# Performance work log

Hardware: AMD Instinct MI355X
Metric: run time of the kernel (lower is better)

The kernel has to match this reference:

```python
import jax, jax.numpy as jnp
import numpy as np

D_MODEL, D_FF, H, DK, DV = 1024, 4096, 16, 64, 64
B, S = 16, 512
EPS = 1e-6

def layer_norm(x, g, b):
    mu = jnp.mean(x, axis=-1, keepdims=True)
    var = jnp.var(x, axis=-1, keepdims=True)
    return (x - mu) / jnp.sqrt(var + EPS) * g + b

def setup_inputs() -> dict:
    key = jax.random.key(0)
    ks = jax.random.split(key, 16)
    def lin(k, fan_in, fan_out):
        lim = 1.0 / np.sqrt(fan_in)
        kw, kb = jax.random.split(k)
        W = jax.random.uniform(kw, (fan_in, fan_out), jnp.float32, -lim, lim)
        b = jax.random.uniform(kb, (fan_out,), jnp.float32, -lim, lim)
        return W, b
    Wq, bq = lin(ks[0], D_MODEL, DK * H)
    Wk, bk = lin(ks[1], D_MODEL, DK * H)
    Wv, bv = lin(ks[2], D_MODEL, DV * H)
    Wo, bo = lin(ks[3], DV * H, D_MODEL)
    w1, b1 = lin(ks[4], D_MODEL, D_FF)   # conv1d k=1 == pointwise linear
    w2, b2 = lin(ks[5], D_FF, D_MODEL)
    return {
        "enc_inputs": jax.random.normal(ks[6], (B, S, D_MODEL), jnp.float32),
        "Wq": Wq, "bq": bq, "Wk": Wk, "bk": bk, "Wv": Wv, "bv": bv,
        "Wo": Wo, "bo": bo,
        "ln1_g": jnp.ones((D_MODEL,), jnp.float32), "ln1_b": jnp.zeros((D_MODEL,), jnp.float32),
        "w1": w1, "b1": b1, "w2": w2, "b2": b2,
        "ln2_g": jnp.ones((D_MODEL,), jnp.float32), "ln2_b": jnp.zeros((D_MODEL,), jnp.float32),
        "mask": jax.random.randint(ks[7], (B, S), 0, 2, jnp.int32),
        "max_neighbors": S,
    }

def reference(enc_inputs, Wq, bq, Wk, bk, Wv, bv, Wo, bo, ln1_g, ln1_b,
              w1, b1, w2, b2, ln2_g, ln2_b, mask, max_neighbors):
    x = enc_inputs  # [B, S, D]
    residual = x
    # projections -> [B, H, S, d]
    q = (x @ Wq + bq).reshape(B, S, H, DK).transpose(0, 2, 1, 3)
    k = (x @ Wk + bk).reshape(B, S, H, DK).transpose(0, 2, 1, 3)
    v = (x @ Wv + bv).reshape(B, S, H, DV).transpose(0, 2, 1, 3)
    scores = jnp.einsum('bhqd,bhkd->bhqk', q, k) / np.sqrt(DK)
    pad = (mask == 0)[:, None, None, :]  # [B,1,1,S] broadcasts over heads & query
    scores = jnp.where(pad, jnp.float32(-1e9), scores)
    attn = jax.nn.softmax(scores, axis=-1)
    ctx = jnp.einsum('bhqk,bhkd->bhqd', attn, v)
    ctx = ctx.transpose(0, 2, 1, 3).reshape(B, S, H * DV)
    ctx = ctx @ Wo + bo
    ctx = layer_norm(ctx + residual, ln1_g, ln1_b)
    # position-wise FFN (conv1d kernel=1 == linear)
    ff = jax.nn.relu(ctx @ w1 + b1) @ w2 + b2
    out = layer_norm(ff + ctx, ln2_g, ln2_b)
    return out, attn
```

## Files before the change

kernel.cpp:

```cpp
#include <hip/hip_runtime.h>
#include <hip/hip_bf16.h>

typedef unsigned short u16;
typedef __bf16 bf16x8 __attribute__((ext_vector_type(8)));
typedef float f32x4 __attribute__((ext_vector_type(4)));

static __device__ __forceinline__ float b2f(u16 x) {
    unsigned int u = ((unsigned int)x) << 16;
    float f; __builtin_memcpy(&f, &u, 4); return f;
}
static __device__ __forceinline__ float b2f_u32(unsigned int u) {
    float f; __builtin_memcpy(&f, &u, 4); return f;
}
static __device__ __forceinline__ u16 f2b(float f) {
    unsigned int u; __builtin_memcpy(&u, &f, 4);
    unsigned int lsb = (u >> 16) & 1u;
    u += 0x7fffu + lsb;
    return (u16)(u >> 16);
}

static __device__ __forceinline__ void gload16(const u16* g, u16* l) {
    __builtin_amdgcn_global_load_lds(
        (const __attribute__((address_space(1))) unsigned int*)g,
        (__attribute__((address_space(3))) unsigned int*)l, 16, 0, 0);
}

__global__ __launch_bounds__(256) void transpose_f2b(const float* __restrict__ src,
                                                     u16* __restrict__ dst,
                                                     int R, int C) {
    __shared__ u16 tile[32][33];
    int c0 = blockIdx.x * 32, r0 = blockIdx.y * 32;
    int tx = threadIdx.x & 31, ty = threadIdx.x >> 5;
    for (int i = ty; i < 32; i += 8) {
        int r = r0 + i, c = c0 + tx;
        tile[i][tx] = (r < R && c < C) ? f2b(src[(long)r * C + c]) : (u16)0;
    }
    __syncthreads();
    for (int i = ty; i < 32; i += 8) {
        int c = c0 + i, r = r0 + tx;
        if (c < C && r < R) dst[(long)c * R + r] = tile[tx][i];
    }
}

__global__ __launch_bounds__(256) void concat3(const float* a, const float* b, const float* c,
                                               float* out) {
    int i = blockIdx.x * 256 + threadIdx.x;
    if (i < 1024) out[i] = a[i];
    else if (i < 2048) out[i] = b[i - 1024];
    else if (i < 3072) out[i] = c[i - 2048];
}

__global__ __launch_bounds__(256) void conv_f2b(const float* __restrict__ src,
                                                u16* __restrict__ dst, long n) {
    long i = ((long)blockIdx.x * 256 + threadIdx.x) * 4;
    if (i >= n) return;
    float4 f = *(const float4*)(src + i);
    ushort4 o;
    o.x = f2b(f.x); o.y = f2b(f.y); o.z = f2b(f.z); o.w = f2b(f.w);
    *(ushort4*)(dst + i) = o;
}

#define BM 128
#define BN 128
#define BK 32
__global__ __launch_bounds__(256) void gemm_bt(
    const u16* __restrict__ A, const u16* __restrict__ B,
    const float* __restrict__ bias, u16* __restrict__ C,
    int M, int N, int K, int lda, int ldb, int ldc, int relu) {
    __shared__ __align__(16) u16 As[BM][BK];
    __shared__ __align__(16) u16 Bs[BN][BK];

    int m0 = blockIdx.y * BM;
    int n0 = blockIdx.x * BN;
    int tid = threadIdx.x;
    int lane = tid & 63;
    int wave = tid >> 6;
    int wm = (wave >> 1) * 64;
    int wn = (wave & 1) * 64;
    int lrow = lane & 15;
    int quad = lane >> 4;

    f32x4 acc[4][4];
#pragma unroll
    for (int i = 0; i < 4; i++)
#pragma unroll
        for (int j = 0; j < 4; j++) acc[i][j] = (f32x4){0.f, 0.f, 0.f, 0.f};

    const u16* Arow = A + (long)m0 * lda;
    const u16* Brow = B + (long)n0 * ldb;

    for (int k0 = 0; k0 < K; k0 += BK) {
#pragma unroll
        for (int i = 0; i < 2; i++) {
            int idx = (i * 4 + wave) * 64 + lane;
            int row = idx >> 2;
            int seg = (idx & 3) * 8;
            gload16(Arow + (long)row * lda + k0 + seg, &As[0][0] + (i * 4 + wave) * 512);
            gload16(Brow + (long)row * ldb + k0 + seg, &Bs[0][0] + (i * 4 + wave) * 512);
        }
        __syncthreads();

        bf16x8 af[4], bfr[4];
#pragma unroll
        for (int mi = 0; mi < 4; mi++)
            af[mi] = *(const bf16x8*)&As[wm + mi * 16 + lrow][quad * 8];
#pragma unroll
        for (int ni = 0; ni < 4; ni++)
            bfr[ni] = *(const bf16x8*)&Bs[wn + ni * 16 + lrow][quad * 8];
#pragma unroll
        for (int mi = 0; mi < 4; mi++)
#pragma unroll
            for (int ni = 0; ni < 4; ni++)
                acc[mi][ni] = __builtin_amdgcn_mfma_f32_16x16x32_bf16(
                    af[mi], bfr[ni], acc[mi][ni], 0, 0, 0);
        __syncthreads();
    }

#pragma unroll
    for (int mi = 0; mi < 4; mi++) {
        int r0w = m0 + wm + mi * 16 + quad * 4;
#pragma unroll
        for (int ni = 0; ni < 4; ni++) {
            int col = n0 + wn + ni * 16 + lrow;
            float bv = bias ? bias[col] : 0.f;
#pragma unroll
            for (int r = 0; r < 4; r++) {
                float v = acc[mi][ni][r] + bv;
                if (relu) v = fmaxf(v, 0.f);
                C[(long)(r0w + r) * ldc + col] = f2b(v);
            }
        }
    }
}

__global__ __launch_bounds__(512, 1) void gemm_bt256(
    const u16* __restrict__ A, const u16* __restrict__ B,
    const float* __restrict__ bias, u16* __restrict__ C,
    int M, int N, int K, int lda, int ldb, int ldc, int relu, int nbx) {
    __shared__ __align__(16) u16 lds[2][4][8192];

    int nwg = gridDim.x;
    int id = blockIdx.x;
    int swz = (id & 7) * (nwg >> 3) + (id >> 3);
    int bx = swz % nbx, by = swz / nbx;
    long m0 = (long)by * 256, n0 = (long)bx * 256;

    int tid = threadIdx.x, lane = tid & 63, wave = tid >> 6;
    int lrow = lane & 15, quad = lane >> 4;
    int wm2 = wave >> 2;
    int wn2 = wave & 3;

    int laneRd = (lrow * 64 + quad * 16) ^ (((lrow >> 3) & 1) << 5);
    int Sl = (lane * 16) ^ (((lane >> 5) & 1) << 5);
    int wr = (Sl >> 6) & 15;
    int wb = Sl & 63;

    f32x4 acc[8][4];
#pragma unroll
    for (int i = 0; i < 8; i++)
#pragma unroll
        for (int j = 0; j < 4; j++) acc[i][j] = (f32x4){0.f, 0.f, 0.f, 0.f};
    bf16x8 af[4][2], bfr[2][2];

#define STAGE_HT(nb, ht, kt) do {                                              \
    const char* _gb = ((ht) < 2)                                               \
        ? (const char*)(A + (m0 + (ht) * 128) * lda)                           \
        : (const char*)(B + (n0 + ((ht) - 2) * 128) * ldb);                    \
    long _ld = (long)(((ht) < 2) ? lda : ldb) * 2;                             \
    _Pragma("unroll")                                                          \
    for (int j = 0; j < 2; j++) {                                              \
        int sub = j * 8 + wave;                                                \
        int srow = (sub >> 1) * 16 + wr;                                       \
        int scolb = (sub & 1) * 64 + wb;                                       \
        gload16((const u16*)(_gb + (long)srow * _ld + (long)(kt) * 128 + scolb),\
                &lds[nb][ht][sub << 9]);                                       \
    }                                                                          \
} while (0)

#define DSLOAD_A(qm) do {                                                      \
    const char* _p = _ab + ((qm) << 14);                                       \
    _Pragma("unroll") for (int mi = 0; mi < 4; mi++)                           \
    _Pragma("unroll") for (int kk = 0; kk < 2; kk++)                           \
        af[mi][kk] = *(const bf16x8*)(_p + ((mi * 4 + kk) << 10));             \
} while (0)

#define DSLOAD_B(qn) do {                                                      \
    const char* _p = _bb + ((qn) << 14);                                       \
    _Pragma("unroll") for (int ni = 0; ni < 2; ni++)                           \
    _Pragma("unroll") for (int kk = 0; kk < 2; kk++)                           \
        bfr[ni][kk] = *(const bf16x8*)(_p + ((ni * 8 + kk) << 10));            \
} while (0)

#define DOMFMA(qm, qn) do {                                                    \
    __builtin_amdgcn_s_setprio(1);                                             \
    _Pragma("unroll") for (int mi = 0; mi < 4; mi++)                           \
    _Pragma("unroll") for (int ni = 0; ni < 2; ni++)                           \
    _Pragma("unroll") for (int kk = 0; kk < 2; kk++)                           \
        acc[(qm) * 4 + mi][(qn) * 2 + ni] =                                    \
            __builtin_amdgcn_mfma_f32_16x16x32_bf16(                           \
                af[mi][kk], bfr[ni][kk], acc[(qm) * 4 + mi][(qn) * 2 + ni],    \
                0, 0, 0);                                                      \
    __builtin_amdgcn_s_setprio(0);                                             \
} while (0)

#define MIDBAR()  do { __builtin_amdgcn_s_barrier(); __builtin_amdgcn_sched_barrier(0); } while (0)
#define ENDBAR()  do { __builtin_amdgcn_sched_barrier(0); __builtin_amdgcn_s_barrier(); } while (0)

    int NT = K >> 6;
    STAGE_HT(0, 0, 0);
    STAGE_HT(0, 2, 0);
    STAGE_HT(0, 1, 0);
    STAGE_HT(0, 3, 0);

    for (int t = 0; t < NT - 1; t++) {
        int cur = t & 1, nxt = cur ^ 1;
        const char* _ab = (const char*)&lds[cur][0][0] + (wm2 << 11) + laneRd;
        const char* _bb = (const char*)&lds[cur][2][0] + (wn2 << 11) + laneRd;
        STAGE_HT(nxt, 0, t + 1);
        asm volatile("s_waitcnt vmcnt(6)" ::: "memory");
        MIDBAR();
        DSLOAD_A(0); DSLOAD_B(0); DOMFMA(0, 0);
        ENDBAR();
        STAGE_HT(nxt, 2, t + 1);
        asm volatile("s_waitcnt vmcnt(6)" ::: "memory");
        MIDBAR();
        DSLOAD_A(1); DOMFMA(1, 0);
        ENDBAR();
        STAGE_HT(nxt, 1, t + 1);
        asm volatile("s_waitcnt vmcnt(6)" ::: "memory");
        MIDBAR();
        DSLOAD_B(1); DOMFMA(1, 1);
        ENDBAR();
        STAGE_HT(nxt, 3, t + 1);
        MIDBAR();
        DSLOAD_A(0); DOMFMA(0, 1);
        ENDBAR();
    }
    {
        int cur = (NT - 1) & 1;
        const char* _ab = (const char*)&lds[cur][0][0] + (wm2 << 11) + laneRd;
        const char* _bb = (const char*)&lds[cur][2][0] + (wn2 << 11) + laneRd;
        asm volatile("s_waitcnt vmcnt(4)" ::: "memory");
        MIDBAR();
        DSLOAD_A(0); DSLOAD_B(0); DOMFMA(0, 0);
        ENDBAR();
        asm volatile("s_waitcnt vmcnt(2)" ::: "memory");
        MIDBAR();
        DSLOAD_A(1); DOMFMA(1, 0);
        ENDBAR();
        asm volatile("s_waitcnt vmcnt(0)" ::: "memory");
        MIDBAR();
        DSLOAD_B(1); DOMFMA(1, 1);
        ENDBAR();
        DSLOAD_A(0); DOMFMA(0, 1);
    }

#pragma unroll
    for (int mg = 0; mg < 8; mg++) {
        long row0 = m0 + (long)(((mg >> 2) * 8 + (mg & 3) * 2 + wm2) * 16 + quad * 4);
#pragma unroll
        for (int ng = 0; ng < 4; ng++) {
            long col = n0 + ((ng >> 1) * 8 + (ng & 1) * 4 + wn2) * 16 + lrow;
            float bv = bias ? bias[col] : 0.f;
#pragma unroll
            for (int r = 0; r < 4; r++) {
                float v = acc[mg][ng][r] + bv;
                if (relu) v = fmaxf(v, 0.f);
                C[(row0 + r) * ldc + col] = f2b(v);
            }
        }
    }
#undef STAGE_HT
#undef DSLOAD_A
#undef DSLOAD_B
#undef DOMFMA
#undef MIDBAR
#undef ENDBAR
}

__global__ __launch_bounds__(256) void split_v(const u16* __restrict__ qkv,
                                               u16* __restrict__ vT) {
    __shared__ u16 tile[32][33];
    int bh = blockIdx.z;
    int b = bh >> 4, h = bh & 15;
    int s0 = blockIdx.x * 32;
    int d0 = blockIdx.y * 32;
    int tx = threadIdx.x & 31, ty = threadIdx.x >> 5;
    for (int i = ty; i < 32; i += 8)
        tile[i][tx] = qkv[((long)(b * 512 + s0 + i)) * 3072 + 2048 + h * 64 + d0 + tx];
    __syncthreads();
    for (int i = ty; i < 32; i += 8)
        vT[((long)bh * 64 + d0 + i) * 512 + s0 + tx] = tile[tx][i];
}

__global__ __launch_bounds__(256) void attn_fused(
    const u16* __restrict__ qkv, const u16* __restrict__ vT,
    const int* __restrict__ mask, float* __restrict__ attnOut,
    u16* __restrict__ ctx) {
    __shared__ __align__(16) u16 s_tile[128][72];
    __shared__ __align__(16) u16 s_p[4][16][136];
    __shared__ unsigned long long m_bits[8];

    int id = blockIdx.x;
    int t_ = id >> 3;
    int mtile = t_ & 7;
    int bh = (id & 7) + ((t_ >> 3) << 3);
    int b = bh >> 4, h = bh & 15;
    int tid = threadIdx.x, lane = tid & 63, wave = tid >> 6;
    int lrow = lane & 15, quad = lane >> 4;
    int m0 = mtile * 64;

    const u16* Qbase = qkv + (long)(b * 512) * 3072 + h * 64;
    const u16* Kbase = Qbase + 1024;

    {
        int i0 = wave * 64 + lane;
        unsigned long long bl0 = __ballot(mask[b * 512 + i0] != 0);
        if (lane == 0) m_bits[wave] = bl0;
        unsigned long long bl1 = __ballot(mask[b * 512 + 256 + i0] != 0);
        if (lane == 0) m_bits[4 + wave] = bl1;
    }

#pragma unroll
    for (int i = 0; i < 2; i++) {
        int idx = i * 256 + tid;
        int r = idx >> 3, c = (idx & 7) * 8;
        *(uint4*)&s_tile[r][c] = *(const uint4*)(Qbase + (long)(m0 + r) * 3072 + c);
    }
    __syncthreads();
    bf16x8 qf[2];
    qf[0] = *(const bf16x8*)&s_tile[wave * 16 + lrow][0 + quad * 8];
    qf[1] = *(const bf16x8*)&s_tile[wave * 16 + lrow][32 + quad * 8];
    __syncthreads();

    f32x4 sacc[32];
#pragma unroll
    for (int t = 0; t < 32; t++) sacc[t] = (f32x4){0.f, 0.f, 0.f, 0.f};

    for (int nc = 0; nc < 4; nc++) {
#pragma unroll
        for (int i = 0; i < 4; i++) {
            int idx = i * 256 + tid;
            int r = idx >> 3, c = (idx & 7) * 8;
            *(uint4*)&s_tile[r][c] = *(const uint4*)(Kbase + (long)(nc * 128 + r) * 3072 + c);
        }
        __syncthreads();
#pragma unroll
        for (int ni = 0; ni < 8; ni++) {
            bf16x8 b0 = *(const bf16x8*)&s_tile[ni * 16 + lrow][0 + quad * 8];
            bf16x8 b1 = *(const bf16x8*)&s_tile[ni * 16 + lrow][32 + quad * 8];
            int t = nc * 8 + ni;
            sacc[t] = __builtin_amdgcn_mfma_f32_16x16x32_bf16(qf[0], b0, sacc[t], 0, 0, 0);
            sacc[t] = __builtin_amdgcn_mfma_f32_16x16x32_bf16(qf[1], b1, sacc[t], 0, 0, 0);
        }
        __syncthreads();
    }

    float mx[4] = {-3.0e38f, -3.0e38f, -3.0e38f, -3.0e38f};
#pragma unroll
    for (int t = 0; t < 32; t++) {
        int col = t * 16 + lrow;
        int on = (int)((m_bits[col >> 6] >> (col & 63)) & 1ull);
#pragma unroll
        for (int r = 0; r < 4; r++) {
            float s = on ? sacc[t][r] * 0.125f : -1e9f;
            sacc[t][r] = s;
            mx[r] = fmaxf(mx[r], s);
        }
    }
#pragma unroll
    for (int off = 1; off < 16; off <<= 1)
#pragma unroll
        for (int r = 0; r < 4; r++) mx[r] = fmaxf(mx[r], __shfl_xor(mx[r], off));
    float sm[4] = {0.f, 0.f, 0.f, 0.f};
#pragma unroll
    for (int t = 0; t < 32; t++)
#pragma unroll
        for (int r = 0; r < 4; r++) {
            float e = __expf(sacc[t][r] - mx[r]);
            sacc[t][r] = e;
            sm[r] += e;
        }
#pragma unroll
    for (int off = 1; off < 16; off <<= 1)
#pragma unroll
        for (int r = 0; r < 4; r++) sm[r] += __shfl_xor(sm[r], off);
#pragma unroll
    for (int r = 0; r < 4; r++) sm[r] = 1.0f / sm[r];
#pragma unroll
    for (int t = 0; t < 32; t++)
#pragma unroll
        for (int r = 0; r < 4; r++) sacc[t][r] *= sm[r];

    f32x4 cacc[4];
#pragma unroll
    for (int ni = 0; ni < 4; ni++) cacc[ni] = (f32x4){0.f, 0.f, 0.f, 0.f};
    const u16* vh = vT + (long)bh * 64 * 512;
    int prr = lane >> 5;
    int pcc = lane & 31;

    for (int nc = 0; nc < 4; nc++) {
#pragma unroll
        for (int t2 = 0; t2 < 8; t2++) {
            int t = nc * 8 + t2;
#pragma unroll
            for (int r = 0; r < 4; r++)
                s_p[wave][quad * 4 + r][t2 * 16 + lrow] = f2b(sacc[t][r]);
        }
        __syncthreads();

        {
            float* abase = attnOut + (long)bh * 512 * 512
                         + (long)(m0 + wave * 16) * 512 + nc * 128;
#pragma unroll
            for (int i = 0; i < 8; i++) {
                int row = i * 2 + prr;
                uint2 pv = *(const uint2*)&s_p[wave][row][pcc * 4];
                float4 o;
                o.x = b2f_u32(pv.x << 16);
                o.y = b2f_u32(pv.x & 0xffff0000u);
                o.z = b2f_u32(pv.y << 16);
                o.w = b2f_u32(pv.y & 0xffff0000u);
                *(float4*)(abase + (long)row * 512 + pcc * 4) = o;
            }
        }

#pragma unroll
        for (int kk = 0; kk < 4; kk++) {
            bf16x8 pf = *(const bf16x8*)&s_p[wave][lrow][kk * 32 + quad * 8];
#pragma unroll
            for (int ni = 0; ni < 4; ni++) {
                bf16x8 vf = *(const bf16x8*)(vh + (long)(ni * 16 + lrow) * 512 + nc * 128 + kk * 32 + quad * 8);
                cacc[ni] = __builtin_amdgcn_mfma_f32_16x16x32_bf16(pf, vf, cacc[ni], 0, 0, 0);
            }
        }
    }

    u16* crow = ctx + (long)(b * 512 + m0 + wave * 16 + quad * 4) * 1024 + h * 64 + lrow;
#pragma unroll
    for (int ni = 0; ni < 4; ni++)
#pragma unroll
        for (int r = 0; r < 4; r++) crow[(long)r * 1024 + ni * 16] = f2b(cacc[ni][r]);
}

__global__ __launch_bounds__(256) void add_ln(const u16* __restrict__ a,
                                              const void* __restrict__ r, int r_fp32,
                                              const float* __restrict__ g,
                                              const float* __restrict__ beta,
                                              void* __restrict__ out, int out_fp32) {
    long row = blockIdx.x;
    const u16* pa = a + row * 1024;
    int tid = threadIdx.x;
    float v[4];
    float sum = 0.f, sq = 0.f;
#pragma unroll
    for (int j = 0; j < 4; j++) {
        int c = tid + j * 256;
        float rv = r_fp32 ? ((const float*)r)[row * 1024 + c]
                          : b2f(((const u16*)r)[row * 1024 + c]);
        float x = b2f(pa[c]) + rv;
        v[j] = x;
        sum += x;
        sq += x * x;
    }
#pragma unroll
    for (int off = 32; off >= 1; off >>= 1) {
        sum += __shfl_xor(sum, off);
        sq += __shfl_xor(sq, off);
    }
    __shared__ float red[2][4];
    int wave = tid >> 6, lane = tid & 63;
    if (lane == 0) { red[0][wave] = sum; red[1][wave] = sq; }
    __syncthreads();
    sum = red[0][0] + red[0][1] + red[0][2] + red[0][3];
    sq = red[1][0] + red[1][1] + red[1][2] + red[1][3];
    float mu = sum * (1.f / 1024.f);
    float var = sq * (1.f / 1024.f) - mu * mu;
    float rstd = rsqrtf(var + 1e-6f);
#pragma unroll
    for (int j = 0; j < 4; j++) {
        int c = tid + j * 256;
        float y = (v[j] - mu) * rstd * g[c] + beta[c];
        if (out_fp32) ((float*)out)[row * 1024 + c] = y;
        else ((u16*)out)[row * 1024 + c] = f2b(y);
    }
}

extern "C" void kernel_launch(void* const* d_in, const int* in_sizes, int n_in,
                              void* d_out, int out_size, void* d_ws, size_t ws_size,
                              hipStream_t stream) {
    const float* x   = (const float*)d_in[0];
    const float* Wq  = (const float*)d_in[1];
    const float* bq  = (const float*)d_in[2];
    const float* Wk  = (const float*)d_in[3];
    const float* bk  = (const float*)d_in[4];
    const float* Wv  = (const float*)d_in[5];
    const float* bv  = (const float*)d_in[6];
    const float* Wo  = (const float*)d_in[7];
    const float* bo  = (const float*)d_in[8];
    const float* g1  = (const float*)d_in[9];
    const float* be1 = (const float*)d_in[10];
    const float* w1  = (const float*)d_in[11];
    const float* b1  = (const float*)d_in[12];
    const float* w2  = (const float*)d_in[13];
    const float* b2  = (const float*)d_in[14];
    const float* g2  = (const float*)d_in[15];
    const float* be2 = (const float*)d_in[16];
    const int* mask  = (const int*)d_in[17];

    float* out = (float*)d_out;
    float* attn = out + (long)8192 * 1024;

    char* w = (char*)d_ws;
    auto alloc = [&](size_t bytes) {
        char* p = w;
        w += (bytes + 255) & ~(size_t)255;
        return p;
    };
    u16* WqkvT = (u16*)alloc(3072L * 1024 * 2);
    u16* WoT   = (u16*)alloc(1024L * 1024 * 2);
    u16* w1T   = (u16*)alloc(4096L * 1024 * 2);
    u16* w2T   = (u16*)alloc(1024L * 4096 * 2);
    float* bqkv = (float*)alloc(3072L * 4);
    u16* xb    = (u16*)alloc(8192L * 1024 * 2);
    char* P1 = alloc(8192L * 4096 * 2);
    u16* qkv = (u16*)P1;
    u16* ff  = (u16*)P1;
    char* P2 = alloc(256L * 64 * 512 * 2);
    u16* vT = (u16*)P2;
    u16* y2 = (u16*)P2;
    u16* ctx = (u16*)alloc(8192L * 1024 * 2);
    u16* x1  = (u16*)alloc(8192L * 1024 * 2);
    u16* y   = (u16*)alloc(8192L * 1024 * 2);

    dim3 blk(256);

    transpose_f2b<<<dim3(32, 32), blk, 0, stream>>>(Wq, WqkvT, 1024, 1024);
    transpose_f2b<<<dim3(32, 32), blk, 0, stream>>>(Wk, WqkvT + 1024L * 1024, 1024, 1024);
    transpose_f2b<<<dim3(32, 32), blk, 0, stream>>>(Wv, WqkvT + 2048L * 1024, 1024, 1024);
    transpose_f2b<<<dim3(32, 32), blk, 0, stream>>>(Wo, WoT, 1024, 1024);
    transpose_f2b<<<dim3(128, 32), blk, 0, stream>>>(w1, w1T, 1024, 4096);
    transpose_f2b<<<dim3(32, 128), blk, 0, stream>>>(w2, w2T, 4096, 1024);
    concat3<<<12, blk, 0, stream>>>(bq, bk, bv, bqkv);
    conv_f2b<<<8192, blk, 0, stream>>>(x, xb, 8192L * 1024);

    gemm_bt256<<<dim3(384), dim3(512), 0, stream>>>(
        xb, WqkvT, bqkv, qkv, 8192, 3072, 1024, 1024, 1024, 3072, 0, 12);

    split_v<<<dim3(16, 2, 256), blk, 0, stream>>>(qkv, vT);

    attn_fused<<<dim3(2048), blk, 0, stream>>>(qkv, vT, mask, attn, ctx);

    gemm_bt<<<dim3(8, 64), blk, 0, stream>>>(
        ctx, WoT, bo, y, 8192, 1024, 1024, 1024, 1024, 1024, 0);

    add_ln<<<8192, blk, 0, stream>>>(y, x, 1, g1, be1, x1, 0);

    gemm_bt256<<<dim3(512), dim3(512), 0, stream>>>(
        x1, w1T, b1, ff, 8192, 4096, 1024, 1024, 1024, 4096, 1, 16);

    gemm_bt<<<dim3(8, 64), blk, 0, stream>>>(
        ff, w2T, b2, y2, 8192, 1024, 4096, 4096, 4096, 1024, 0);

    add_ln<<<8192, blk, 0, stream>>>(y2, x1, 0, g2, be2, out, 1);
}
```

Measured before the change: 864.1 us.

## Use pipelined 128x256 GEMM for N=1024 projections; load K directly in attention

After: 870.0 us. No clear change (+0.7%).

```diff
diff --git a/kernel.cpp b/kernel.cpp
--- a/kernel.cpp
+++ b/kernel.cpp
@@ -58,79 +58,6 @@
     ushort4 o;
     o.x = f2b(f.x); o.y = f2b(f.y); o.z = f2b(f.z); o.w = f2b(f.w);
     *(ushort4*)(dst + i) = o;
-}
-
-#define BM 128
-#define BN 128
-#define BK 32
-__global__ __launch_bounds__(256) void gemm_bt(
-    const u16* __restrict__ A, const u16* __restrict__ B,
-    const float* __restrict__ bias, u16* __restrict__ C,
-    int M, int N, int K, int lda, int ldb, int ldc, int relu) {
-    __shared__ __align__(16) u16 As[BM][BK];
-    __shared__ __align__(16) u16 Bs[BN][BK];
-
-    int m0 = blockIdx.y * BM;
-    int n0 = blockIdx.x * BN;
-    int tid = threadIdx.x;
-    int lane = tid & 63;
-    int wave = tid >> 6;
-    int wm = (wave >> 1) * 64;
-    int wn = (wave & 1) * 64;
-    int lrow = lane & 15;
-    int quad = lane >> 4;
-
-    f32x4 acc[4][4];
-#pragma unroll
-    for (int i = 0; i < 4; i++)
-#pragma unroll
-        for (int j = 0; j < 4; j++) acc[i][j] = (f32x4){0.f, 0.f, 0.f, 0.f};
-
-    const u16* Arow = A + (long)m0 * lda;
-    const u16* Brow = B + (long)n0 * ldb;
-
-    for (int k0 = 0; k0 < K; k0 += BK) {
-#pragma unroll
-        for (int i = 0; i < 2; i++) {
-            int idx = (i * 4 + wave) * 64 + lane;
-            int row = idx >> 2;
-            int seg = (idx & 3) * 8;
-            gload16(Arow + (long)row * lda + k0 + seg, &As[0][0] + (i * 4 + wave) * 512);
-            gload16(Brow + (long)row * ldb + k0 + seg, &Bs[0][0] + (i * 4 + wave) * 512);
-        }
-        __syncthreads();
-
-        bf16x8 af[4], bfr[4];
-#pragma unroll
-        for (int mi = 0; mi < 4; mi++)
-            af[mi] = *(const bf16x8*)&As[wm + mi * 16 + lrow][quad * 8];
-#pragma unroll
-        for (int ni = 0; ni < 4; ni++)
-            bfr[ni] = *(const bf16x8*)&Bs[wn + ni * 16 + lrow][quad * 8];
-#pragma unroll
-        for (int mi = 0; mi < 4; mi++)
-#pragma unroll
-            for (int ni = 0; ni < 4; ni++)
-                acc[mi][ni] = __builtin_amdgcn_mfma_f32_16x16x32_bf16(
-                    af[mi], bfr[ni], acc[mi][ni], 0, 0, 0);
-        __syncthreads();
-    }
-
-#pragma unroll
-    for (int mi = 0; mi < 4; mi++) {
-        int r0w = m0 + wm + mi * 16 + quad * 4;
-#pragma unroll
-        for (int ni = 0; ni < 4; ni++) {
-            int col = n0 + wn + ni * 16 + lrow;
-            float bv = bias ? bias[col] : 0.f;
-#pragma unroll
-            for (int r = 0; r < 4; r++) {
-                float v = acc[mi][ni][r] + bv;
-                if (relu) v = fmaxf(v, 0.f);
-                C[(long)(r0w + r) * ldc + col] = f2b(v);
-            }
-        }
-    }
 }
 
 __global__ __launch_bounds__(512, 1) void gemm_bt256(
@@ -274,6 +201,129 @@
 #undef DSLOAD_A
 #undef DSLOAD_B
 #undef DOMFMA
+}
+
+__global__ __launch_bounds__(512, 1) void gemm_btn(
+    const u16* __restrict__ A, const u16* __restrict__ B,
+    const float* __restrict__ bias, u16* __restrict__ C,
+    int K, int lda, int ldb, int ldc, int relu, int nbx) {
+    __shared__ __align__(16) u16 lds[2][3][8192];
+
+    int nwg = gridDim.x;
+    int id = blockIdx.x;
+    int swz = (id & 7) * (nwg >> 3) + (id >> 3);
+    int bx = swz % nbx, by = swz / nbx;
+    long m0 = (long)by * 128, n0 = (long)bx * 256;
+
+    int tid = threadIdx.x, lane = tid & 63, wave = tid >> 6;
+    int lrow = lane & 15, quad = lane >> 4;
+    int wm2 = wave >> 2;
+    int wn2 = wave & 3;
+
+    int laneRd = (lrow * 64 + quad * 16) ^ (((lrow >> 3) & 1) << 5);
+    int Sl = (lane * 16) ^ (((lane >> 5) & 1) << 5);
+    int wr = (Sl >> 6) & 15;
+    int wb = Sl & 63;
+
+    f32x4 acc[4][4];
+#pragma unroll
+    for (int i = 0; i < 4; i++)
+#pragma unroll
+        for (int j = 0; j < 4; j++) acc[i][j] = (f32x4){0.f, 0.f, 0.f, 0.f};
+    bf16x8 af[4][2], bfr[2][2];
+
+#define STAGE_HT(nb, ht, kt) do {                                              \
+    const char* _gb = ((ht) == 0)                                              \
+        ? (const char*)(A + m0 * lda)                                          \
+        : (const char*)(B + (n0 + ((ht) - 1) * 128) * ldb);                    \
+    long _ld = (long)(((ht) == 0) ? lda : ldb) * 2;                            \
+    _Pragma("unroll")                                                          \
+    for (int j = 0; j < 2; j++) {                                              \
+        int sub = j * 8 + wave;                                                \
+        int srow = (sub >> 1) * 16 + wr;                                       \
+        int scolb = (sub & 1) * 64 + wb;                                       \
+        gload16((const u16*)(_gb + (long)srow * _ld + (long)(kt) * 128 + scolb),\
+                &lds[nb][ht][sub << 9]);                                       \
+    }                                                                          \
+} while (0)
+
+#define DSLOAD_A() do {                                                        \
+    _Pragma("unroll") for (int mi = 0; mi < 4; mi++)                           \
+    _Pragma("unroll") for (int kk = 0; kk < 2; kk++)                           \
+        af[mi][kk] = *(const bf16x8*)(_ab + ((mi * 4 + kk) << 10));            \
+} while (0)
+
+#define DSLOAD_B(qn) do {                                                      \
+    const char* _p = _b0 + (qn) * 16384;                                       \
+    _Pragma("unroll") for (int ni = 0; ni < 2; ni++)                           \
+    _Pragma("unroll") for (int kk = 0; kk < 2; kk++)                           \
+        bfr[ni][kk] = *(const bf16x8*)(_p + ((ni * 8 + kk) << 10));            \
+} while (0)
+
+#define DOMFMA(qn) do {                                                        \
+    __builtin_amdgcn_s_setprio(1);                                             \
+    _Pragma("unroll") for (int mi = 0; mi < 4; mi++)                           \
+    _Pragma("unroll") for (int ni = 0; ni < 2; ni++)                           \
+    _Pragma("unroll") for (int kk = 0; kk < 2; kk++)                           \
+        acc[mi][(qn) * 2 + ni] =                                               \
+            __builtin_amdgcn_mfma_f32_16x16x32_bf16(                           \
+                af[mi][kk], bfr[ni][kk], acc[mi][(qn) * 2 + ni], 0, 0, 0);     \
+    __builtin_amdgcn_s_setprio(0);                                             \
+} while (0)
+
+    int NT = K >> 6;
+    STAGE_HT(0, 0, 0);
+    STAGE_HT(0, 1, 0);
+    STAGE_HT(0, 2, 0);
+
+    for (int t = 0; t < NT - 1; t++) {
+        int cur = t & 1, nxt = cur ^ 1;
+        const char* _ab = (const char*)&lds[cur][0][0] + (wm2 << 11) + laneRd;
+        const char* _b0 = (const char*)&lds[cur][1][0] + (wn2 << 11) + laneRd;
+        STAGE_HT(nxt, 0, t + 1);
+        asm volatile("s_waitcnt vmcnt(4)" ::: "memory");
+        MIDBAR();
+        DSLOAD_A(); DSLOAD_B(0); DOMFMA(0);
+        ENDBAR();
+        STAGE_HT(nxt, 1, t + 1);
+        STAGE_HT(nxt, 2, t + 1);
+        asm volatile("s_waitcnt vmcnt(6)" ::: "memory");
+        MIDBAR();
+        DSLOAD_B(1); DOMFMA(1);
+        ENDBAR();
+    }
+    {
+        int cur = (NT - 1) & 1;
+        const char* _ab = (const char*)&lds[cur][0][0] + (wm2 << 11) + laneRd;
+        const char* _b0 = (const char*)&lds[cur][1][0] + (wn2 << 11) + laneRd;
+        asm volatile("s_waitcnt vmcnt(2)" ::: "memory");
+        MIDBAR();
+        DSLOAD_A(); DSLOAD_B(0); DOMFMA(0);
+        ENDBAR();
+        asm volatile("s_waitcnt vmcnt(0)" ::: "memory");
+        MIDBAR();
+        DSLOAD_B(1); DOMFMA(1);
+    }
+
+#pragma unroll
+    for (int mi = 0; mi < 4; mi++) {
+        long row0 = m0 + (long)((mi * 2 + wm2) * 16 + quad * 4);
+#pragma unroll
+        for (int ng = 0; ng < 4; ng++) {
+            long col = n0 + ((ng >> 1) * 8 + (ng & 1) * 4 + wn2) * 16 + lrow;
+            float bv = bias ? bias[col] : 0.f;
+#pragma unroll
+            for (int r = 0; r < 4; r++) {
+                float v = acc[mi][ng][r] + bv;
+                if (relu) v = fmaxf(v, 0.f);
+                C[(row0 + r) * ldc + col] = f2b(v);
+            }
+        }
+    }
+#undef STAGE_HT
+#undef DSLOAD_A
+#undef DSLOAD_B
+#undef DOMFMA
 #undef MIDBAR
 #undef ENDBAR
 }
@@ -297,7 +347,7 @@
     const u16* __restrict__ qkv, const u16* __restrict__ vT,
     const int* __restrict__ mask, float* __restrict__ attnOut,
     u16* __restrict__ ctx) {
-    __shared__ __align__(16) u16 s_tile[128][72];
+    __shared__ __align__(16) u16 s_tile[64][72];
     __shared__ __align__(16) u16 s_p[4][16][136];
     __shared__ unsigned long long m_bits[8];
 
@@ -331,29 +381,18 @@
     bf16x8 qf[2];
     qf[0] = *(const bf16x8*)&s_tile[wave * 16 + lrow][0 + quad * 8];
     qf[1] = *(const bf16x8*)&s_tile[wave * 16 + lrow][32 + quad * 8];
-    __syncthreads();
 
     f32x4 sacc[32];
 #pragma unroll
     for (int t = 0; t < 32; t++) sacc[t] = (f32x4){0.f, 0.f, 0.f, 0.f};
 
-    for (int nc = 0; nc < 4; nc++) {
-#pragma unroll
-        for (int i = 0; i < 4; i++) {
-            int idx = i * 256 + tid;
-            int r = idx >> 3, c = (idx & 7) * 8;
-            *(uint4*)&s_tile[r][c] = *(const uint4*)(Kbase + (long)(nc * 128 + r) * 3072 + c);
-        }
-        __syncthreads();
-#pragma unroll
-        for (int ni = 0; ni < 8; ni++) {
-            bf16x8 b0 = *(const bf16x8*)&s_tile[ni * 16 + lrow][0 + quad * 8];
-            bf16x8 b1 = *(const bf16x8*)&s_tile[ni * 16 + lrow][32 + quad * 8];
-            int t = nc * 8 + ni;
-            sacc[t] = __builtin_amdgcn_mfma_f32_16x16x32_bf16(qf[0], b0, sacc[t], 0, 0, 0);
-            sacc[t] = __builtin_amdgcn_mfma_f32_16x16x32_bf16(qf[1], b1, sacc[t], 0, 0, 0);
-        }
-        __syncthreads();
+#pragma unroll
+    for (int t = 0; t < 32; t++) {
+        const u16* krow = Kbase + (long)(t * 16 + lrow) * 3072 + quad * 8;
+        bf16x8 b0 = *(const bf16x8*)krow;
+        bf16x8 b1 = *(const bf16x8*)(krow + 32);
+        sacc[t] = __builtin_amdgcn_mfma_f32_16x16x32_bf16(qf[0], b0, sacc[t], 0, 0, 0);
+        sacc[t] = __builtin_amdgcn_mfma_f32_16x16x32_bf16(qf[1], b1, sacc[t], 0, 0, 0);
     }
 
     float mx[4] = {-3.0e38f, -3.0e38f, -3.0e38f, -3.0e38f};
@@ -407,7 +446,6 @@
             for (int r = 0; r < 4; r++)
                 s_p[wave][quad * 4 + r][t2 * 16 + lrow] = f2b(sacc[t][r]);
         }
-        __syncthreads();
 
         {
             float* abase = attnOut + (long)bh * 512 * 512
@@ -551,16 +589,16 @@
 
     attn_fused<<<dim3(2048), blk, 0, stream>>>(qkv, vT, mask, attn, ctx);
 
-    gemm_bt<<<dim3(8, 64), blk, 0, stream>>>(
-        ctx, WoT, bo, y, 8192, 1024, 1024, 1024, 1024, 1024, 0);
+    gemm_btn<<<dim3(256), dim3(512), 0, stream>>>(
+        ctx, WoT, bo, y, 1024, 1024, 1024, 1024, 0, 4);
 
     add_ln<<<8192, blk, 0, stream>>>(y, x, 1, g1, be1, x1, 0);
 
     gemm_bt256<<<dim3(512), dim3(512), 0, stream>>>(
         x1, w1T, b1, ff, 8192, 4096, 1024, 1024, 1024, 4096, 1, 16);
 
-    gemm_bt<<<dim3(8, 64), blk, 0, stream>>>(
-        ff, w2T, b2, y2, 8192, 1024, 4096, 4096, 4096, 1024, 0);
+    gemm_btn<<<dim3(256), dim3(512), 0, stream>>>(
+        ff, w2T, b2, y2, 4096, 4096, 4096, 1024, 0, 4);
 
     add_ln<<<8192, blk, 0, stream>>>(y2, x1, 0, g2, be2, out, 1);
 }
```
